# Kernel optimization log

Measured on AMD Instinct MI355X. Metric: run time of the kernel, lower is better.

Reference implementation:

```python
import jax, jax.numpy as jnp
import numpy as np

B, N, C = 1, 256, 128        # batch, n_res, norm_channel
H, AC = 4, 32                # num_head, attention_channel


def setup_inputs() -> dict:
    key = jax.random.key(0)
    ks = jax.random.split(key, 9)
    s = 0.02
    return {
        "act": jax.random.normal(ks[0], (B, N, N, C), jnp.float32),
        "mask": jnp.ones((B, N, N), jnp.float32),
        "ln_g": jnp.ones((C,), jnp.float32),
        "ln_b": jnp.zeros((C,), jnp.float32),
        "wq": (jax.random.normal(ks[1], (C, H * AC), jnp.float32) * s),
        "wk": (jax.random.normal(ks[2], (C, H * AC), jnp.float32) * s),
        "wv": (jax.random.normal(ks[3], (C, H * AC), jnp.float32) * s),
        "w2d": (jax.random.normal(ks[4], (C, H), jnp.float32) * s),
        "wg": (jax.random.normal(ks[5], (C, H * AC), jnp.float32) * s),
        "bg": jnp.zeros((H * AC,), jnp.float32),
        "wo": (jax.random.normal(ks[6], (H * AC, C), jnp.float32) * s),
        "bo": jnp.zeros((C,), jnp.float32),
    }


def reference(act, mask, ln_g, ln_b, wq, wk, wv, w2d, wg, bg, wo, bo):
    eps = 1e-5
    mu = jnp.mean(act, axis=-1, keepdims=True)
    var = jnp.mean(jnp.square(act - mu), axis=-1, keepdims=True)
    a = (act - mu) * jax.lax.rsqrt(var + eps) * ln_g + ln_b  # LayerNorm

    b_, m_, i_, _ = a.shape
    q = (a @ wq).reshape(b_, m_, i_, H, AC)
    k = (a @ wk).reshape(b_, m_, i_, H, AC)
    v = (a @ wv).reshape(b_, m_, i_, H, AC)

    factor = 1.0 / np.sqrt(AC).astype(np.float32)
    # mask bias: [b, m, 1, 1, j]
    bias = (1e9 * (mask - 1.0))[:, :, None, None, :]
    aff = jnp.einsum('bmihc,bmjhc->bmhij', q * factor, k) + bias

    # pair bias: [b, h, i, j], broadcast over m (torch trailing-dim broadcast, b=1)
    nb = jnp.einsum('bijc,ch->bhij', a, w2d)
    weights = jax.nn.softmax(aff + nb[:, None], axis=-1)  # [b,m,h,i,j]

    g = jax.nn.sigmoid(a @ wg + bg).reshape(b_, m_, i_, H, AC)
    out = jnp.einsum('bmhqk,bmkhc->bmqhc', weights, v) * g  # [b,m,q,h,c]
    return out.reshape(b_, m_, i_, H * AC) @ wo + bo
```

## Files before the change

kernel.cpp:

```cpp
#include <hip/hip_runtime.h>
#include <hip/hip_fp16.h>
#include <math.h>


#define NRES 256
#define CCH  128
#define NROWS (NRES * NRES)
#define FACTOR 0.17677669529663687f

typedef __attribute__((ext_vector_type(8))) __bf16 bf16x8;
typedef __attribute__((ext_vector_type(4))) float f32x4;

__device__ __forceinline__ f32x4 mfma16(bf16x8 a, bf16x8 b, f32x4 c) {
    return __builtin_amdgcn_mfma_f32_16x16x32_bf16(a, b, c, 0, 0, 0);
}

union PK4 { __bf16 b[4]; uint2 u2; };
union PK2 { __bf16 b[2]; unsigned int u; };

__device__ __forceinline__ void hilo(float x, __bf16& h, __bf16& l) {
    h = (__bf16)x;
    l = (__bf16)(x - (float)h);
}

__global__ __launch_bounds__(256) void prep_kernel(
    const float* __restrict__ wq, const float* __restrict__ wk,
    const float* __restrict__ wv, const float* __restrict__ wg,
    const float* __restrict__ wo,
    __bf16* __restrict__ wph, __bf16* __restrict__ wpl)
{
    const int gid = blockIdx.x * 256 + threadIdx.x;
    const int wid = gid >> 11;
    const int rem = gid & 2047;
    const int nstrip = rem >> 8;
    const int kf = (rem >> 6) & 3;
    const int lane = rem & 63;
    const int l15 = lane & 15, quad = lane >> 4;
    const float* W = (wid == 0) ? wq : (wid == 1) ? wk :
                     (wid == 2) ? wv : (wid == 3) ? wg : wo;
    const float scale = (wid == 0) ? FACTOR : 1.0f;
    bf16x8 hb, lb;
    #pragma unroll
    for (int e = 0; e < 8; ++e) {
        int k = kf * 32 + quad * 8 + e;
        int n = nstrip * 16 + l15;
        float v = W[k * CCH + n] * scale;
        __bf16 h, l; hilo(v, h, l);
        hb[e] = h; lb[e] = l;
    }
    *(bf16x8*)&wph[(size_t)gid * 8] = hb;
    *(bf16x8*)&wpl[(size_t)gid * 8] = lb;
}

__global__ __launch_bounds__(256) void lnproj_kernel(
    const float* __restrict__ act, const float* __restrict__ ln_g,
    const float* __restrict__ ln_b, const float* __restrict__ w2d,
    const __bf16* __restrict__ wph, const float* __restrict__ bg,
    __bf16* __restrict__ qb, __bf16* __restrict__ kb,
    __bf16* __restrict__ vb, __half* __restrict__ gfh,
    float* __restrict__ nbP)
{
    __shared__ __align__(16) char smem[26112];
    __bf16* const aH = (__bf16*)smem;
    const int t = threadIdx.x, w = t >> 6, lane = t & 63;
    const int l15 = lane & 15, quad = lane >> 4;
    const int r0 = blockIdx.x * 32;

    {
        const int ridx = t >> 3, g = t & 7;
        const int grow = r0 + ridx;
        const float* __restrict__ xp = act + (size_t)grow * CCH + g * 16;
        float4 x4[4];
        #pragma unroll
        for (int c = 0; c < 4; ++c) x4[c] = *(const float4*)(xp + c * 4);
        float s = 0.f, sq = 0.f;
        #pragma unroll
        for (int c = 0; c < 4; ++c) {
            s  += (x4[c].x + x4[c].y) + (x4[c].z + x4[c].w);
            sq += x4[c].x * x4[c].x + x4[c].y * x4[c].y +
                  x4[c].z * x4[c].z + x4[c].w * x4[c].w;
        }
        #pragma unroll
        for (int o = 1; o <= 4; o <<= 1) {
            s  += __shfl_xor(s, o, 64);
            sq += __shfl_xor(sq, o, 64);
        }
        float mu  = s * (1.0f / CCH);
        float var = fmaf(sq, 1.0f / CCH, -mu * mu);
        float rs  = rsqrtf(var + 1e-5f);
        float av[16];
        #pragma unroll
        for (int c = 0; c < 4; ++c) {
            float4 g4 = *(const float4*)&ln_g[g * 16 + c * 4];
            float4 b4 = *(const float4*)&ln_b[g * 16 + c * 4];
            float* xv = (float*)&x4[c];
            float* gv = (float*)&g4;
            float* bv = (float*)&b4;
            #pragma unroll
            for (int e = 0; e < 4; ++e)
                av[c * 4 + e] = fmaf((xv[e] - mu) * rs, gv[e], bv[e]);
        }
        #pragma unroll
        for (int p = 0; p < 8; ++p) {
            PK2 ph;
            ph.b[0] = (__bf16)av[p * 2];
            ph.b[1] = (__bf16)av[p * 2 + 1];
            *(unsigned int*)&aH[ridx * 136 + g * 16 + p * 2] = ph.u;
        }
        float nb[4] = {0.f, 0.f, 0.f, 0.f};
        const float4* __restrict__ w2d4 = (const float4*)w2d;
        #pragma unroll
        for (int c = 0; c < 16; ++c) {
            float4 wv = w2d4[g * 16 + c];
            nb[0] = fmaf(av[c], wv.x, nb[0]);
            nb[1] = fmaf(av[c], wv.y, nb[1]);
            nb[2] = fmaf(av[c], wv.z, nb[2]);
            nb[3] = fmaf(av[c], wv.w, nb[3]);
        }
        #pragma unroll
        for (int o = 1; o <= 4; o <<= 1)
            #pragma unroll
            for (int hh = 0; hh < 4; ++hh)
                nb[hh] += __shfl_xor(nb[hh], o, 64);
        if (g == 0) {
            const int i = grow >> 8, j = grow & 255;
            #pragma unroll
            for (int hh = 0; hh < 4; ++hh) {
                size_t f = ((size_t)hh << 14) + ((size_t)(i >> 4) << 10) +
                           ((size_t)(j >> 4) << 6) + ((size_t)((j >> 2) & 3) << 4) +
                           (i & 15);
                nbP[f * 4 + (j & 3)] = nb[hh];
            }
        }
    }
    __syncthreads();

    const int tensor = w;
    const __bf16* __restrict__ Bh = wph + (size_t)tensor * 16384;
    f32x4 acc0[8], acc1[8];
    #pragma unroll
    for (int n = 0; n < 8; ++n) {
        acc0[n] = (f32x4){0.f, 0.f, 0.f, 0.f};
        acc1[n] = (f32x4){0.f, 0.f, 0.f, 0.f};
    }
    #pragma unroll
    for (int kf = 0; kf < 4; ++kf) {
        const int ao = l15 * 136 + kf * 32 + quad * 8;
        bf16x8 A0 = *(const bf16x8*)&aH[ao];
        bf16x8 A1 = *(const bf16x8*)&aH[ao + 16 * 136];
        #pragma unroll
        for (int n = 0; n < 8; ++n) {
            bf16x8 bh = *(const bf16x8*)&Bh[(size_t)((n * 4 + kf) * 64 + lane) * 8];
            acc0[n] = mfma16(A0, bh, acc0[n]);
            acc1[n] = mfma16(A1, bh, acc1[n]);
        }
    }

    char* const stg = smem + 8704 + w * 4352;
    if (tensor == 3) {
        __half* const sth = (__half*)stg;
        #pragma unroll 1
        for (int s = 0; s < 2; ++s) {
            f32x4* accp = s ? acc1 : acc0;
            #pragma unroll
            for (int n = 0; n < 8; ++n)
                #pragma unroll
                for (int r = 0; r < 4; ++r) {
                    float v = accp[n][r] + bg[n * 16 + l15];
                    sth[(quad * 4 + r) * 136 + n * 16 + l15] =
                        (__half)(1.0f / (1.0f + __expf(-v)));
                }
            #pragma unroll
            for (int i = 0; i < 4; ++i) {
                int row = i * 4 + (lane >> 4);
                int c8 = lane & 15;
                uint4 hv = *(const uint4*)&sth[row * 136 + c8 * 8];
                *(uint4*)&gfh[(size_t)(r0 + s * 16 + row) * CCH + c8 * 8] = hv;
            }
        }
    } else {
        __bf16* const sth = (__bf16*)stg;
        __bf16* const oh = (tensor == 0) ? qb : (tensor == 1) ? kb : vb;
        #pragma unroll 1
        for (int s = 0; s < 2; ++s) {
            f32x4* accp = s ? acc1 : acc0;
            #pragma unroll
            for (int n = 0; n < 8; ++n)
                #pragma unroll
                for (int r = 0; r < 4; ++r)
                    sth[(quad * 4 + r) * 136 + n * 16 + l15] = (__bf16)accp[n][r];
            #pragma unroll
            for (int i = 0; i < 4; ++i) {
                int row = i * 4 + (lane >> 4);
                int c8 = lane & 15;
                uint4 hv = *(const uint4*)&sth[row * 136 + c8 * 8];
                *(uint4*)&oh[(size_t)(r0 + s * 16 + row) * CCH + c8 * 8] = hv;
            }
        }
    }
}

__global__ __launch_bounds__(256) void attn_kernel(
    const __bf16* __restrict__ qb, const __bf16* __restrict__ kb,
    const __bf16* __restrict__ vb, const __half* __restrict__ gfh,
    const float* __restrict__ mask, const float* __restrict__ nbP,
    __bf16* __restrict__ gth, __bf16* __restrict__ gtl)
{
    __shared__ __align__(16) char smem[23040];
    __bf16* const vth = (__bf16*)smem;
    __bf16* const pbb = (__bf16*)(smem + 16896);
    float*  const biasrow = (float*)(smem + 22016);
    const int t = threadIdx.x, w = t >> 6, lane = t & 63;
    const int l15 = lane & 15, quad = lane >> 4;
    const int mrow = blockIdx.x >> 2, h = blockIdx.x & 3;
    const size_t rbase = (size_t)mrow * NRES;
    const int ch0 = h * 32;

    biasrow[t] = 1e9f * (mask[mrow * NRES + t] - 1.0f);

    #pragma unroll
    for (int it = 0; it < 4; ++it) {
        int f = t + it * 256;
        int j = f >> 2, cg = f & 3;
        bf16x8 hv = *(const bf16x8*)&vb[(rbase + j) * CCH + ch0 + cg * 8];
        #pragma unroll
        for (int e = 0; e < 8; ++e)
            vth[(cg * 8 + e) * 264 + j] = hv[e];
    }
    __syncthreads();

    const int i0 = w * 64;
    bf16x8 Qh[4];
    #pragma unroll
    for (int s = 0; s < 4; ++s)
        Qh[s] = *(const bf16x8*)&qb[(rbase + i0 + s * 16 + l15) * CCH + ch0 + quad * 8];

    f32x4 O[4][2];
    float ls[4] = {0.f, 0.f, 0.f, 0.f};
    #pragma unroll
    for (int s = 0; s < 4; ++s) {
        O[s][0] = (f32x4){0.f, 0.f, 0.f, 0.f};
        O[s][1] = (f32x4){0.f, 0.f, 0.f, 0.f};
    }
    __bf16* const ph = pbb + w * 640;

    for (int jb = 0; jb < NRES; jb += 32) {
        bf16x8 Kh[2];
        #pragma unroll
        for (int js = 0; js < 2; ++js)
            Kh[js] = *(const bf16x8*)&kb[(rbase + jb + js * 16 + l15) * CCH + ch0 + quad * 8];
        bf16x8 Vh2[2];
        #pragma unroll
        for (int c = 0; c < 2; ++c)
            Vh2[c] = *(const bf16x8*)&vth[(c * 16 + l15) * 264 + jb + quad * 8];
        #pragma unroll
        for (int s = 0; s < 4; ++s) {
            #pragma unroll
            for (int js = 0; js < 2; ++js) {
                f32x4 S = (f32x4){0.f, 0.f, 0.f, 0.f};
                S = mfma16(Kh[js], Qh[s], S);
                size_t f4 = (((size_t)(h * 16 + w * 4 + s) * 16 +
                              (jb >> 4) + js) << 6) + quad * 16 + l15;
                float4 nb4 = *(const float4*)&nbP[f4 * 4];
                float4 mb4 = *(const float4*)&biasrow[jb + js * 16 + quad * 4];
                float p0 = __expf(S[0] + nb4.x + mb4.x - 4.0f);
                float p1 = __expf(S[1] + nb4.y + mb4.y - 4.0f);
                float p2 = __expf(S[2] + nb4.z + mb4.z - 4.0f);
                float p3 = __expf(S[3] + nb4.w + mb4.w - 4.0f);
                ls[s] += (p0 + p1) + (p2 + p3);
                PK4 hh;
                hh.b[0] = (__bf16)p0; hh.b[1] = (__bf16)p1;
                hh.b[2] = (__bf16)p2; hh.b[3] = (__bf16)p3;
                *(uint2*)&ph[l15 * 40 + js * 16 + quad * 4] = hh.u2;
            }
            bf16x8 Ph = *(const bf16x8*)&ph[l15 * 40 + quad * 8];
            #pragma unroll
            for (int c = 0; c < 2; ++c)
                O[s][c] = mfma16(Vh2[c], Ph, O[s][c]);
        }
    }

    #pragma unroll
    for (int s = 0; s < 4; ++s) {
        ls[s] += __shfl_xor(ls[s], 16, 64);
        ls[s] += __shfl_xor(ls[s], 32, 64);
    }

    float ov[4][2][4];
    #pragma unroll
    for (int s = 0; s < 4; ++s) {
        float inv = 1.0f / ls[s];
        #pragma unroll
        for (int c = 0; c < 2; ++c) {
            size_t gi = (rbase + i0 + s * 16 + l15) * CCH + ch0 + c * 16 + quad * 4;
            uint2 gu = *(const uint2*)&gfh[gi];
            const __half* gh = (const __half*)&gu;
            #pragma unroll
            for (int r = 0; r < 4; ++r)
                ov[s][c][r] = O[s][c][r] * inv * (float)gh[r];
        }
    }
    __syncthreads();
    __bf16* const stp = (__bf16*)(smem + w * 5120);
    #pragma unroll
    for (int s = 0; s < 4; ++s)
        #pragma unroll
        for (int c = 0; c < 2; ++c) {
            PK4 hh;
            #pragma unroll
            for (int r = 0; r < 4; ++r) hh.b[r] = (__bf16)ov[s][c][r];
            *(uint2*)&stp[(s * 16 + l15) * 40 + c * 16 + quad * 4] = hh.u2;
        }
    #pragma unroll
    for (int i = 0; i < 4; ++i) {
        int row = i * 16 + (lane >> 2);
        int c8 = lane & 3;
        uint4 hv = *(const uint4*)&stp[row * 40 + c8 * 8];
        *(uint4*)&gth[(rbase + i0 + row) * CCH + ch0 + c8 * 8] = hv;
    }
    #pragma unroll
    for (int s = 0; s < 4; ++s)
        #pragma unroll
        for (int c = 0; c < 2; ++c) {
            PK4 ll;
            #pragma unroll
            for (int r = 0; r < 4; ++r) {
                __bf16 hv = (__bf16)ov[s][c][r];
                ll.b[r] = (__bf16)(ov[s][c][r] - (float)hv);
            }
            *(uint2*)&stp[(s * 16 + l15) * 40 + c * 16 + quad * 4] = ll.u2;
        }
    #pragma unroll
    for (int i = 0; i < 4; ++i) {
        int row = i * 16 + (lane >> 2);
        int c8 = lane & 3;
        uint4 lv = *(const uint4*)&stp[row * 40 + c8 * 8];
        *(uint4*)&gtl[(rbase + i0 + row) * CCH + ch0 + c8 * 8] = lv;
    }
}

__global__ __launch_bounds__(256) void out_kernel(
    const __bf16* __restrict__ gth, const __bf16* __restrict__ gtl,
    const __bf16* __restrict__ wph, const __bf16* __restrict__ wpl,
    const float* __restrict__ bo, float* __restrict__ out)
{
    __shared__ __align__(16) float eps[4][16 * 132];
    const int t = threadIdx.x, w = t >> 6, lane = t & 63;
    const int l15 = lane & 15, quad = lane >> 4;
    const int r0 = blockIdx.x * 64 + w * 16;
    const __bf16* __restrict__ Bh = wph + (size_t)4 * 16384;
    const __bf16* __restrict__ Bl = wpl + (size_t)4 * 16384;

    f32x4 acc[8];
    #pragma unroll
    for (int n = 0; n < 8; ++n) acc[n] = (f32x4){0.f, 0.f, 0.f, 0.f};

    #pragma unroll
    for (int kf = 0; kf < 4; ++kf) {
        size_t idx = (size_t)(r0 + l15) * CCH + kf * 32 + quad * 8;
        bf16x8 Ahf = *(const bf16x8*)&gth[idx];
        bf16x8 Alf = *(const bf16x8*)&gtl[idx];
        #pragma unroll
        for (int n = 0; n < 8; ++n) {
            size_t boff = (size_t)((n * 4 + kf) * 64 + lane) * 8;
            bf16x8 bh = *(const bf16x8*)&Bh[boff];
            bf16x8 bl = *(const bf16x8*)&Bl[boff];
            acc[n] = mfma16(Ahf, bh, acc[n]);
            acc[n] = mfma16(Ahf, bl, acc[n]);
            acc[n] = mfma16(Alf, bh, acc[n]);
        }
    }

    #pragma unroll
    for (int n = 0; n < 8; ++n)
        #pragma unroll
        for (int r = 0; r < 4; ++r)
            eps[w][(quad * 4 + r) * 132 + n * 16 + l15] = acc[n][r];
    const int erow = lane >> 2;
    const int ecg0 = lane & 3;
    #pragma unroll
    for (int it = 0; it < 8; ++it) {
        int cg = ecg0 + it * 4;
        float4 v4 = *(const float4*)&eps[w][erow * 132 + cg * 4];
        float4 b4 = *(const float4*)&bo[cg * 4];
        v4.x += b4.x; v4.y += b4.y; v4.z += b4.z; v4.w += b4.w;
        *(float4*)&out[(size_t)(r0 + erow) * CCH + cg * 4] = v4;
    }
}

extern "C" void kernel_launch(void* const* d_in, const int* in_sizes, int n_in,
                              void* d_out, int out_size, void* d_ws, size_t ws_size,
                              hipStream_t stream)
{
    const float* act  = (const float*)d_in[0];
    const float* mask = (const float*)d_in[1];
    const float* ln_g = (const float*)d_in[2];
    const float* ln_b = (const float*)d_in[3];
    const float* wq   = (const float*)d_in[4];
    const float* wk   = (const float*)d_in[5];
    const float* wv   = (const float*)d_in[6];
    const float* w2d  = (const float*)d_in[7];
    const float* wg   = (const float*)d_in[8];
    const float* bg   = (const float*)d_in[9];
    const float* wo   = (const float*)d_in[10];
    const float* bo   = (const float*)d_in[11];
    float* out = (float*)d_out;

    const size_t SZ = (size_t)NROWS * CCH;
    __bf16* bws = (__bf16*)d_ws;
    __bf16* qb  = bws;
    __bf16* kb  = bws + SZ;
    __bf16* vb  = bws + 2 * SZ;
    __bf16* gth = bws + 3 * SZ;
    __bf16* gtl = bws + 4 * SZ;
    __half* gfh = (__half*)(bws + 5 * SZ);
    float* nbP = (float*)(bws + 6 * SZ);
    __bf16* wph = (__bf16*)(nbP + 4 * NROWS);
    __bf16* wpl = wph + 5 * 16384;

    prep_kernel<<<40, 256, 0, stream>>>(wq, wk, wv, wg, wo, wph, wpl);
    lnproj_kernel<<<2048, 256, 0, stream>>>(
        act, ln_g, ln_b, w2d, wph, bg, qb, kb, vb, gfh, nbP);
    attn_kernel<<<NRES * 4, 256, 0, stream>>>(
        qb, kb, vb, gfh, mask, nbP, gth, gtl);
    out_kernel<<<1024, 256, 0, stream>>>(gth, gtl, wph, wpl, bo, out);
}
```

Measured before the change: 204.5 us.

## Make each wave own 32 rows and compute all four projections in lnproj

The LayerNorm+projection kernel is restructured so each wave normalises its own 32 rows into a private LDS tile and loops over the q, k, v and gate weight tensors. Previously each block shared one 32-row tile across four waves, one tensor per wave. This removes the block-wide __syncthreads and lets the LN, pair-bias and bf16 packing use two lanes per row with wider loads. The grid shrinks 4x and each wave does serial work over four tensors with more registers live, which may cut occupancy and latency hiding.

```diff
diff --git a/kernel.cpp b/kernel.cpp
--- a/kernel.cpp
+++ b/kernel.cpp
@@ -60,69 +60,61 @@
     __bf16* __restrict__ vb, __half* __restrict__ gfh,
     float* __restrict__ nbP)
 {
-    __shared__ __align__(16) char smem[26112];
-    __bf16* const aH = (__bf16*)smem;
+    __shared__ __align__(16) char smem[34816];
     const int t = threadIdx.x, w = t >> 6, lane = t & 63;
     const int l15 = lane & 15, quad = lane >> 4;
-    const int r0 = blockIdx.x * 32;
+    __bf16* const aH = (__bf16*)(smem + w * 8704);
+    const int r0w = blockIdx.x * 128 + w * 32;
 
     {
-        const int ridx = t >> 3, g = t & 7;
-        const int grow = r0 + ridx;
-        const float* __restrict__ xp = act + (size_t)grow * CCH + g * 16;
-        float4 x4[4];
-        #pragma unroll
-        for (int c = 0; c < 4; ++c) x4[c] = *(const float4*)(xp + c * 4);
+        const int row = lane >> 1, half = lane & 1;
+        const int grow = r0w + row;
+        const float* __restrict__ xp = act + (size_t)grow * CCH + half * 64;
+        float4 x4[16];
+        #pragma unroll
+        for (int c = 0; c < 16; ++c) x4[c] = *(const float4*)(xp + c * 4);
         float s = 0.f, sq = 0.f;
         #pragma unroll
-        for (int c = 0; c < 4; ++c) {
+        for (int c = 0; c < 16; ++c) {
             s  += (x4[c].x + x4[c].y) + (x4[c].z + x4[c].w);
             sq += x4[c].x * x4[c].x + x4[c].y * x4[c].y +
                   x4[c].z * x4[c].z + x4[c].w * x4[c].w;
         }
-        #pragma unroll
-        for (int o = 1; o <= 4; o <<= 1) {
-            s  += __shfl_xor(s, o, 64);
-            sq += __shfl_xor(sq, o, 64);
-        }
+        s  += __shfl_xor(s, 1, 64);
+        sq += __shfl_xor(sq, 1, 64);
         float mu  = s * (1.0f / CCH);
         float var = fmaf(sq, 1.0f / CCH, -mu * mu);
         float rs  = rsqrtf(var + 1e-5f);
-        float av[16];
-        #pragma unroll
-        for (int c = 0; c < 4; ++c) {
-            float4 g4 = *(const float4*)&ln_g[g * 16 + c * 4];
-            float4 b4 = *(const float4*)&ln_b[g * 16 + c * 4];
-            float* xv = (float*)&x4[c];
-            float* gv = (float*)&g4;
-            float* bv = (float*)&b4;
-            #pragma unroll
-            for (int e = 0; e < 4; ++e)
-                av[c * 4 + e] = fmaf((xv[e] - mu) * rs, gv[e], bv[e]);
-        }
-        #pragma unroll
-        for (int p = 0; p < 8; ++p) {
-            PK2 ph;
-            ph.b[0] = (__bf16)av[p * 2];
-            ph.b[1] = (__bf16)av[p * 2 + 1];
-            *(unsigned int*)&aH[ridx * 136 + g * 16 + p * 2] = ph.u;
-        }
         float nb[4] = {0.f, 0.f, 0.f, 0.f};
         const float4* __restrict__ w2d4 = (const float4*)w2d;
         #pragma unroll
-        for (int c = 0; c < 16; ++c) {
-            float4 wv = w2d4[g * 16 + c];
-            nb[0] = fmaf(av[c], wv.x, nb[0]);
-            nb[1] = fmaf(av[c], wv.y, nb[1]);
-            nb[2] = fmaf(av[c], wv.z, nb[2]);
-            nb[3] = fmaf(av[c], wv.w, nb[3]);
-        }
-        #pragma unroll
-        for (int o = 1; o <= 4; o <<= 1)
-            #pragma unroll
-            for (int hh = 0; hh < 4; ++hh)
-                nb[hh] += __shfl_xor(nb[hh], o, 64);
-        if (g == 0) {
+        for (int c2 = 0; c2 < 8; ++c2) {
+            bf16x8 pk;
+            #pragma unroll
+            for (int cc = 0; cc < 2; ++cc) {
+                const int c = c2 * 2 + cc;
+                float4 g4 = *(const float4*)&ln_g[half * 64 + c * 4];
+                float4 b4 = *(const float4*)&ln_b[half * 64 + c * 4];
+                float* xv = (float*)&x4[c];
+                float* gv = (float*)&g4;
+                float* bv = (float*)&b4;
+                #pragma unroll
+                for (int e = 0; e < 4; ++e) {
+                    float av = fmaf((xv[e] - mu) * rs, gv[e], bv[e]);
+                    pk[cc * 4 + e] = (__bf16)av;
+                    float4 wv = w2d4[half * 64 + c * 4 + e];
+                    nb[0] = fmaf(av, wv.x, nb[0]);
+                    nb[1] = fmaf(av, wv.y, nb[1]);
+                    nb[2] = fmaf(av, wv.z, nb[2]);
+                    nb[3] = fmaf(av, wv.w, nb[3]);
+                }
+            }
+            *(bf16x8*)&aH[row * 136 + half * 64 + c2 * 8] = pk;
+        }
+        #pragma unroll
+        for (int hh = 0; hh < 4; ++hh)
+            nb[hh] += __shfl_xor(nb[hh], 1, 64);
+        if (half == 0) {
             const int i = grow >> 8, j = grow & 255;
             #pragma unroll
             for (int hh = 0; hh < 4; ++hh) {
@@ -133,68 +125,72 @@
             }
         }
     }
-    __syncthreads();
-
-    const int tensor = w;
-    const __bf16* __restrict__ Bh = wph + (size_t)tensor * 16384;
-    f32x4 acc0[8], acc1[8];
-    #pragma unroll
-    for (int n = 0; n < 8; ++n) {
-        acc0[n] = (f32x4){0.f, 0.f, 0.f, 0.f};
-        acc1[n] = (f32x4){0.f, 0.f, 0.f, 0.f};
-    }
+
+    bf16x8 A0[4], A1[4];
     #pragma unroll
     for (int kf = 0; kf < 4; ++kf) {
         const int ao = l15 * 136 + kf * 32 + quad * 8;
-        bf16x8 A0 = *(const bf16x8*)&aH[ao];
-        bf16x8 A1 = *(const bf16x8*)&aH[ao + 16 * 136];
+        A0[kf] = *(const bf16x8*)&aH[ao];
+        A1[kf] = *(const bf16x8*)&aH[ao + 16 * 136];
+    }
+
+    #pragma unroll 1
+    for (int tn = 0; tn < 4; ++tn) {
+        const __bf16* __restrict__ Bh = wph + (size_t)tn * 16384;
+        f32x4 acc0[8], acc1[8];
         #pragma unroll
         for (int n = 0; n < 8; ++n) {
-            bf16x8 bh = *(const bf16x8*)&Bh[(size_t)((n * 4 + kf) * 64 + lane) * 8];
-            acc0[n] = mfma16(A0, bh, acc0[n]);
-            acc1[n] = mfma16(A1, bh, acc1[n]);
-        }
-    }
-
-    char* const stg = smem + 8704 + w * 4352;
-    if (tensor == 3) {
-        __half* const sth = (__half*)stg;
-        #pragma unroll 1
-        for (int s = 0; s < 2; ++s) {
-            f32x4* accp = s ? acc1 : acc0;
-            #pragma unroll
-            for (int n = 0; n < 8; ++n)
+            acc0[n] = (f32x4){0.f, 0.f, 0.f, 0.f};
+            acc1[n] = (f32x4){0.f, 0.f, 0.f, 0.f};
+        }
+        #pragma unroll
+        for (int kf = 0; kf < 4; ++kf)
+            #pragma unroll
+            for (int n = 0; n < 8; ++n) {
+                bf16x8 bh = *(const bf16x8*)&Bh[(size_t)((n * 4 + kf) * 64 + lane) * 8];
+                acc0[n] = mfma16(A0[kf], bh, acc0[n]);
+                acc1[n] = mfma16(A1[kf], bh, acc1[n]);
+            }
+
+        if (tn == 3) {
+            __half* const sth = (__half*)aH;
+            #pragma unroll 1
+            for (int sp = 0; sp < 2; ++sp) {
+                f32x4* accp = sp ? acc1 : acc0;
                 #pragma unroll
-                for (int r = 0; r < 4; ++r) {
-                    float v = accp[n][r] + bg[n * 16 + l15];
-                    sth[(quad * 4 + r) * 136 + n * 16 + l15] =
-                        (__half)(1.0f / (1.0f + __expf(-v)));
+                for (int n = 0; n < 8; ++n)
+                    #pragma unroll
+                    for (int r = 0; r < 4; ++r) {
+                        float v = accp[n][r] + bg[n * 16 + l15];
+                        sth[(quad * 4 + r) * 136 + n * 16 + l15] =
+                            (__half)(1.0f / (1.0f + __expf(-v)));
+                    }
+                #pragma unroll
+                for (int i = 0; i < 4; ++i) {
+                    int row = i * 4 + (lane >> 4);
+                    int c8 = lane & 15;
+                    uint4 hv = *(const uint4*)&sth[row * 136 + c8 * 8];
+                    *(uint4*)&gfh[(size_t)(r0w + sp * 16 + row) * CCH + c8 * 8] = hv;
                 }
-            #pragma unroll
-            for (int i = 0; i < 4; ++i) {
-                int row = i * 4 + (lane >> 4);
-                int c8 = lane & 15;
-                uint4 hv = *(const uint4*)&sth[row * 136 + c8 * 8];
-                *(uint4*)&gfh[(size_t)(r0 + s * 16 + row) * CCH + c8 * 8] = hv;
-            }
-        }
-    } else {
-        __bf16* const sth = (__bf16*)stg;
-        __bf16* const oh = (tensor == 0) ? qb : (tensor == 1) ? kb : vb;
-        #pragma unroll 1
-        for (int s = 0; s < 2; ++s) {
-            f32x4* accp = s ? acc1 : acc0;
-            #pragma unroll
-            for (int n = 0; n < 8; ++n)
+            }
+        } else {
+            __bf16* const sth = (__bf16*)aH;
+            __bf16* const oh = (tn == 0) ? qb : (tn == 1) ? kb : vb;
+            #pragma unroll 1
+            for (int sp = 0; sp < 2; ++sp) {
+                f32x4* accp = sp ? acc1 : acc0;
                 #pragma unroll
-                for (int r = 0; r < 4; ++r)
-                    sth[(quad * 4 + r) * 136 + n * 16 + l15] = (__bf16)accp[n][r];
-            #pragma unroll
-            for (int i = 0; i < 4; ++i) {
-                int row = i * 4 + (lane >> 4);
-                int c8 = lane & 15;
-                uint4 hv = *(const uint4*)&sth[row * 136 + c8 * 8];
-                *(uint4*)&oh[(size_t)(r0 + s * 16 + row) * CCH + c8 * 8] = hv;
+                for (int n = 0; n < 8; ++n)
+                    #pragma unroll
+                    for (int r = 0; r < 4; ++r)
+                        sth[(quad * 4 + r) * 136 + n * 16 + l15] = (__bf16)accp[n][r];
+                #pragma unroll
+                for (int i = 0; i < 4; ++i) {
+                    int row = i * 4 + (lane >> 4);
+                    int c8 = lane & 15;
+                    uint4 hv = *(const uint4*)&sth[row * 136 + c8 * 8];
+                    *(uint4*)&oh[(size_t)(r0w + sp * 16 + row) * CCH + c8 * 8] = hv;
+                }
             }
         }
     }
@@ -419,7 +415,7 @@
     __bf16* wpl = wph + 5 * 16384;
 
     prep_kernel<<<40, 256, 0, stream>>>(wq, wk, wv, wg, wo, wph, wpl);
-    lnproj_kernel<<<2048, 256, 0, stream>>>(
+    lnproj_kernel<<<512, 256, 0, stream>>>(
         act, ln_g, ln_b, w2d, wph, bg, qb, kb, vb, gfh, nbP);
     attn_kernel<<<NRES * 4, 256, 0, stream>>>(
         qb, kb, vb, gfh, mask, nbP, gth, gtl);
```

Measured after the change: 204.7 us. Within noise of the previous version (+0.1%).
